# Kernel tuning notes

Hardware: AMD Instinct MI355X
Metric: run time of the kernel (lower is better)

Reference implementation:

```python
import jax, jax.numpy as jnp
import numpy as np

N_SRC0, N_DST0, N_DST1 = 100000, 50000, 25000
E0, E1, D = 1600000, 800000, 128


def setup_inputs() -> dict:
    key = jax.random.key(0)
    k = jax.random.split(key, 8)
    return {
        "x": jax.random.normal(k[0], (N_SRC0, D), dtype=jnp.float32),
        "src0": jax.random.randint(k[1], (E0,), 0, N_SRC0, dtype=jnp.int32),
        "dst0": jax.random.randint(k[2], (E0,), 0, N_DST0, dtype=jnp.int32),
        "ew0": jax.random.uniform(k[3], (E0,), dtype=jnp.float32),
        "src1": jax.random.randint(k[4], (E1,), 0, N_DST0, dtype=jnp.int32),
        "dst1": jax.random.randint(k[5], (E1,), 0, N_DST1, dtype=jnp.int32),
        "ew1": jax.random.uniform(k[6], (E1,), dtype=jnp.float32),
        "n_dst0": N_DST0,
        "n_dst1": N_DST1,
    }


def _propagate(h, src, dst, ew, n_dst):
    # u_mul_e: gather src feature per edge and scale by edge weight; sum-reduce to dst
    m = h[src] * ew[:, None]                      # [E, D]
    return jax.ops.segment_sum(m, dst, num_segments=n_dst)  # [n_dst, D]


def reference(x, src0, dst0, ew0, src1, dst1, ew1, n_dst0, n_dst1):
    # LightGCN forward over 2 sampled blocks, mlp_list=None
    h = _propagate(x, src0, dst0, ew0, n_dst0)    # [n_dst0, D]
    h = _propagate(h, src1, dst1, ew1, n_dst1)    # [n_dst1, D]
    return h
```

## Files before the change

kernel.cpp:

```cpp
#include <hip/hip_runtime.h>


#define DIMS 128
#define BK   64
#define BKSH 6
#define CAP  4096
#define CH   8192

__device__ __forceinline__ unsigned bf16_1(float a) {
  unsigned u = __float_as_uint(a);
  return (u + 0x7fffu + ((u >> 16) & 1u)) >> 16;
}

__device__ __forceinline__ int chunk_swz(int b, int NW) {
  const int q = NW >> 3, r = NW & 7, x = b & 7;
  return (x < r ? x * (q + 1) : r * (q + 1) + (x - r) * q) + (b >> 3);
}

__global__ __launch_bounds__(256) void hist_cvt(
    const int* __restrict__ dst0, const int* __restrict__ dst1,
    const float* __restrict__ xf, uint2* __restrict__ xq,
    float* __restrict__ xscale,
    int* __restrict__ wgcnt0, int* __restrict__ wgcnt1,
    int E0, int E1, int NB0, int NB1, int NW0, int NW1, int NSRC) {
  int b = blockIdx.x;
  if (b < NW0 + NW1) {
    __shared__ int hist[1024];
    const int s1 = (b >= NW0);
    const int w  = s1 ? chunk_swz(b - NW0, NW1) : chunk_swz(b, NW0);
    const int E  = s1 ? E1 : E0;
    const int NB = s1 ? NB1 : NB0;
    const int* dst = s1 ? dst1 : dst0;
    int* wgcnt = s1 ? wgcnt1 : wgcnt0;
    for (int i = threadIdx.x; i < NB; i += 256) hist[i] = 0;
    __syncthreads();
    const int beg = w * CH, end = min(beg + CH, E);
    for (int e = beg + threadIdx.x; e < end; e += 256)
      atomicAdd(&hist[dst[e] >> BKSH], 1);
    __syncthreads();
    for (int i = threadIdx.x; i < NB; i += 256)
      wgcnt[w * NB + i] = hist[i];
  } else {
    int gi = (b - NW0 - NW1) * 256 + threadIdx.x;
    int row = gi >> 4, c = gi & 15;
    if (row < NSRC) {
      const float4* xf4 = (const float4*)xf;
      float4 v0 = xf4[(size_t)row * 32 + c * 2];
      float4 v1 = xf4[(size_t)row * 32 + c * 2 + 1];
      float m = fmaxf(fmaxf(fmaxf(fabsf(v0.x), fabsf(v0.y)),
                            fmaxf(fabsf(v0.z), fabsf(v0.w))),
                      fmaxf(fmaxf(fabsf(v1.x), fabsf(v1.y)),
                            fmaxf(fabsf(v1.z), fabsf(v1.w))));
      m = fmaxf(m, __shfl_xor(m, 1));
      m = fmaxf(m, __shfl_xor(m, 2));
      m = fmaxf(m, __shfl_xor(m, 4));
      m = fmaxf(m, __shfl_xor(m, 8));
      float inv = (m > 0.f) ? 127.0f / m : 0.f;
      int q0 = (int)rintf(v0.x * inv), q1 = (int)rintf(v0.y * inv);
      int q2 = (int)rintf(v0.z * inv), q3 = (int)rintf(v0.w * inv);
      int q4 = (int)rintf(v1.x * inv), q5 = (int)rintf(v1.y * inv);
      int q6 = (int)rintf(v1.z * inv), q7 = (int)rintf(v1.w * inv);
      unsigned lo = (q0 & 255) | ((q1 & 255) << 8) |
                    ((q2 & 255) << 16) | ((q3 & 255) << 24);
      unsigned hi = (q4 & 255) | ((q5 & 255) << 8) |
                    ((q6 & 255) << 16) | ((q7 & 255) << 24);
      xq[(size_t)row * 16 + c] = make_uint2(lo, hi);
      if (c == 0) xscale[row] = m * (1.0f / 127.0f);
    }
  }
}

__global__ __launch_bounds__(256) void scan_cols(
    int* __restrict__ wgcnt0, int* __restrict__ wgcnt1,
    int* __restrict__ gcur, int2* __restrict__ rg0, int2* __restrict__ rg1,
    int NB0, int NB1, int NW0, int NW1) {
  __shared__ int part[256];
  int b = blockIdx.x;
  const int s1 = (b >= NB0);
  const int i = s1 ? b - NB0 : b;
  int* wgcnt = s1 ? wgcnt1 : wgcnt0;
  int2* rg   = s1 ? rg1 : rg0;
  const int NB = s1 ? NB1 : NB0;
  const int NW = s1 ? NW1 : NW0;
  const int t = threadIdx.x;
  int v = (t < NW) ? wgcnt[t * NB + i] : 0;
  part[t] = v;
  __syncthreads();
  for (int off = 1; off < 256; off <<= 1) {
    int u = (t >= off) ? part[t - off] : 0;
    __syncthreads();
    part[t] += u;
    __syncthreads();
  }
  if (t < NW) wgcnt[t * NB + i] = part[t] - v;
  if (t == 255) {
    int tot = part[255];
    int base = atomicAdd(&gcur[s1], tot);
    rg[i] = make_int2(base, base + tot);
  }
}

__global__ __launch_bounds__(512) void partition_k(
    const int* __restrict__ src0, const int* __restrict__ dst0,
    const float* __restrict__ ew0, const int* __restrict__ src1,
    const int* __restrict__ dst1, const float* __restrict__ ew1,
    const int* __restrict__ wgcnt0, const int* __restrict__ wgcnt1,
    const int2* __restrict__ rg0, const int2* __restrict__ rg1,
    int2* __restrict__ payl0, int2* __restrict__ payl1,
    int E0, int E1, int NB0, int NB1, int NW0, int NW1) {
  __shared__ int cur[1024];
  int b = blockIdx.x;
  const int s1 = (b >= NW0);
  const int w  = s1 ? chunk_swz(b - NW0, NW1) : chunk_swz(b, NW0);
  const int E  = s1 ? E1 : E0;
  const int NB = s1 ? NB1 : NB0;
  const int* src = s1 ? src1 : src0;
  const int* dst = s1 ? dst1 : dst0;
  const float* ew = s1 ? ew1 : ew0;
  const int* wgcnt = s1 ? wgcnt1 : wgcnt0;
  const int2* rg = s1 ? rg1 : rg0;
  int2* payl = s1 ? payl1 : payl0;
  for (int i = threadIdx.x; i < NB; i += 512)
    cur[i] = rg[i].x + wgcnt[w * NB + i];
  __syncthreads();
  const int beg = w * CH, end = min(beg + CH, E);
  for (int e = beg + threadIdx.x; e < end; e += 512) {
    int d = dst[e];
    int pos = atomicAdd(&cur[d >> BKSH], 1);
    payl[pos] = make_int2(src[e],
                          (int)((bf16_1(ew[e]) << 16) | (unsigned)(d & (BK - 1))));
  }
}

#define EDGE_BLOCK8(ws, u)                                      \
  {                                                             \
    a0 += (float)((int)((u).x << 24) >> 24) * (ws);             \
    a1 += (float)((int)((u).x << 16) >> 24) * (ws);             \
    a2 += (float)((int)((u).x << 8) >> 24) * (ws);              \
    a3 += (float)((int)(u).x >> 24) * (ws);                     \
    a4 += (float)((int)((u).y << 24) >> 24) * (ws);             \
    a5 += (float)((int)((u).y << 16) >> 24) * (ws);             \
    a6 += (float)((int)((u).y << 8) >> 24) * (ws);              \
    a7 += (float)((int)(u).y >> 24) * (ws);                     \
  }

template <bool OUT_I8>
__global__ __launch_bounds__(512) void gather_bkt(
    const uint2* __restrict__ feat, const float* __restrict__ scl,
    const int2* __restrict__ rg, const int2* __restrict__ payl,
    void* __restrict__ outp, float* __restrict__ oscale, int n_dst) {
  __shared__ int2 lp[CAP];
  __shared__ int cnt[BK], base[BK], cnt2[BK];
  const int b = blockIdx.x;
  const int tid = threadIdx.x;
  const int2 r = rg[b];
  const int n = r.y - r.x;
  const int nin = min(n, CAP);
  if (tid < BK) { cnt[tid] = 0; cnt2[tid] = 0; }
  __syncthreads();
  for (int j = tid; j < nin; j += 512)
    atomicAdd(&cnt[payl[r.x + j].y & (BK - 1)], 1);
  __syncthreads();
  if (tid < 64) {
    int v = cnt[tid];
    int s = v;
    for (int off = 1; off < 64; off <<= 1) {
      int u = __shfl_up(s, off);
      if (tid >= off) s += u;
    }
    base[tid] = s - v;
  }
  __syncthreads();
  for (int j = tid; j < nin; j += 512) {
    int2 p = payl[r.x + j];
    int dl = p.y & (BK - 1);
    float ws = __uint_as_float((unsigned)p.y & 0xffff0000u) * scl[p.x];
    int pos = base[dl] + atomicAdd(&cnt2[dl], 1);
    lp[pos] = make_int2(p.x, (int)((bf16_1(ws) << 16) | (unsigned)dl));
  }
  __syncthreads();
  const int wave = tid >> 6;
  const int lane = tid & 63;
  const int rr = lane >> 4;
  const int c  = lane & 15;
  for (int dl = wave; dl < BK; dl += 8) {
    const int row = b * BK + dl;
    if (row >= n_dst) break;
    const int bg = base[dl];
    const int en = bg + cnt[dl];
    float a0 = 0.f, a1 = 0.f, a2 = 0.f, a3 = 0.f;
    float a4 = 0.f, a5 = 0.f, a6 = 0.f, a7 = 0.f;
    for (int j = bg; j < en; j += 4) {
      int jj = j + rr;
      int2 p = (jj < en) ? lp[jj] : make_int2(0, 0);
      float ws = __uint_as_float((unsigned)p.y & 0xffff0000u);
      uint2 u = feat[(size_t)p.x * 16 + c];
      EDGE_BLOCK8(ws, u);
    }
    if (n > CAP) {
      for (int j = CAP; j < n; j += 4) {
        int jj = j + rr;
        int2 p = (jj < n) ? payl[r.x + jj] : make_int2(0, 0);
        bool mine = (jj < n) && ((p.y & (BK - 1)) == dl);
        float ws = mine
            ? __uint_as_float((unsigned)p.y & 0xffff0000u) * scl[p.x] : 0.f;
        uint2 u = feat[(size_t)p.x * 16 + c];
        EDGE_BLOCK8(ws, u);
      }
    }
    a0 += __shfl_xor(a0, 16); a0 += __shfl_xor(a0, 32);
    a1 += __shfl_xor(a1, 16); a1 += __shfl_xor(a1, 32);
    a2 += __shfl_xor(a2, 16); a2 += __shfl_xor(a2, 32);
    a3 += __shfl_xor(a3, 16); a3 += __shfl_xor(a3, 32);
    a4 += __shfl_xor(a4, 16); a4 += __shfl_xor(a4, 32);
    a5 += __shfl_xor(a5, 16); a5 += __shfl_xor(a5, 32);
    a6 += __shfl_xor(a6, 16); a6 += __shfl_xor(a6, 32);
    a7 += __shfl_xor(a7, 16); a7 += __shfl_xor(a7, 32);
    if (OUT_I8) {
      float m = fmaxf(fmaxf(fmaxf(fabsf(a0), fabsf(a1)),
                            fmaxf(fabsf(a2), fabsf(a3))),
                      fmaxf(fmaxf(fabsf(a4), fabsf(a5)),
                            fmaxf(fabsf(a6), fabsf(a7))));
      m = fmaxf(m, __shfl_xor(m, 1));
      m = fmaxf(m, __shfl_xor(m, 2));
      m = fmaxf(m, __shfl_xor(m, 4));
      m = fmaxf(m, __shfl_xor(m, 8));
      m = fmaxf(m, __shfl_xor(m, 16));
      m = fmaxf(m, __shfl_xor(m, 32));
      float inv = (m > 0.f) ? 127.0f / m : 0.f;
      if (rr == 0) {
        int q0 = (int)rintf(a0 * inv), q1 = (int)rintf(a1 * inv);
        int q2 = (int)rintf(a2 * inv), q3 = (int)rintf(a3 * inv);
        int q4 = (int)rintf(a4 * inv), q5 = (int)rintf(a5 * inv);
        int q6 = (int)rintf(a6 * inv), q7 = (int)rintf(a7 * inv);
        unsigned lo = (q0 & 255) | ((q1 & 255) << 8) |
                      ((q2 & 255) << 16) | ((q3 & 255) << 24);
        unsigned hi = (q4 & 255) | ((q5 & 255) << 8) |
                      ((q6 & 255) << 16) | ((q7 & 255) << 24);
        ((uint2*)outp)[(size_t)row * 16 + c] = make_uint2(lo, hi);
      }
      if (lane == 0) oscale[row] = m * (1.0f / 127.0f);
    } else {
      if (rr < 2) {
        ((float4*)outp)[(size_t)row * 32 + c * 2 + rr] =
            (rr == 0) ? make_float4(a0, a1, a2, a3)
                      : make_float4(a4, a5, a6, a7);
      }
    }
  }
}

#define COLG 32
__global__ __launch_bounds__(256) void prop_atomic(
    const float* __restrict__ x, const int* __restrict__ src,
    const int* __restrict__ dst, const float* __restrict__ ew,
    float* __restrict__ out, int E) {
  long long idx = (long long)blockIdx.x * blockDim.x + threadIdx.x;
  long long total = (long long)E * COLG;
  if (idx >= total) return;
  int e = (int)(idx >> 5);
  int cg = (int)(idx & 31);
  int s = src[e];
  int d = dst[e];
  float w = ew[e];
  const float4 v = *reinterpret_cast<const float4*>(x + (size_t)s * DIMS + cg * 4);
  float* o = out + (size_t)d * DIMS + cg * 4;
  atomicAdd(o + 0, v.x * w);
  atomicAdd(o + 1, v.y * w);
  atomicAdd(o + 2, v.z * w);
  atomicAdd(o + 3, v.w * w);
}


static inline size_t align_up(size_t v, size_t a) { return (v + a - 1) / a * a; }

extern "C" void kernel_launch(void* const* d_in, const int* in_sizes, int n_in,
                              void* d_out, int out_size, void* d_ws, size_t ws_size,
                              hipStream_t stream) {
  const float* x    = (const float*)d_in[0];
  const int*   src0 = (const int*)d_in[1];
  const int*   dst0 = (const int*)d_in[2];
  const float* ew0  = (const float*)d_in[3];
  const int*   src1 = (const int*)d_in[4];
  const int*   dst1 = (const int*)d_in[5];
  const float* ew1  = (const float*)d_in[6];

  const int N_SRC0 = in_sizes[0] / DIMS;
  const int E0 = in_sizes[1];
  const int E1 = in_sizes[4];
  const int N_DST0 = 50000;
  const int N_DST1 = 25000;

  const int NB0 = (N_DST0 + BK - 1) / BK;
  const int NB1 = (N_DST1 + BK - 1) / BK;
  const int NW0 = (E0 + CH - 1) / CH;
  const int NW1 = (E1 + CH - 1) / CH;

  float* out = (float*)d_out;

  char* ws = (char*)d_ws;
  size_t off = 0;
  uint2* xq     = (uint2*)(ws + off); off = align_up(off + (size_t)N_SRC0 * 16 * 8, 16);
  float* xscale = (float*)(ws + off); off = align_up(off + (size_t)N_SRC0 * 4, 16);
  uint2* hq     = (uint2*)(ws + off); off = align_up(off + (size_t)N_DST0 * 16 * 8, 16);
  float* hscale = (float*)(ws + off); off = align_up(off + (size_t)N_DST0 * 4, 16);
  int* wgcnt0   = (int*)(ws + off);   off = align_up(off + (size_t)NW0 * NB0 * 4, 16);
  int* wgcnt1   = (int*)(ws + off);   off = align_up(off + (size_t)NW1 * NB1 * 4, 16);
  int* gcur     = (int*)(ws + off);   off = align_up(off + 2 * 4, 16);
  int2* rg0     = (int2*)(ws + off);  off = align_up(off + (size_t)NB0 * 8, 16);
  int2* rg1     = (int2*)(ws + off);  off = align_up(off + (size_t)NB1 * 8, 16);
  int2* payl0   = (int2*)(ws + off);  off = align_up(off + (size_t)E0 * 8, 16);
  int2* payl1   = (int2*)(ws + off);  off = align_up(off + (size_t)E1 * 8, 16);
  const size_t needed = off;

  if (ws_size < needed) {
    float* h = (float*)d_ws;
    hipMemsetAsync(h, 0, (size_t)N_DST0 * DIMS * 4, stream);
    hipMemsetAsync(out, 0, (size_t)N_DST1 * DIMS * 4, stream);
    long long t0 = (long long)E0 * COLG;
    prop_atomic<<<(int)((t0 + 255) / 256), 256, 0, stream>>>(x, src0, dst0, ew0, h, E0);
    long long t1 = (long long)E1 * COLG;
    prop_atomic<<<(int)((t1 + 255) / 256), 256, 0, stream>>>(h, src1, dst1, ew1, out, E1);
    return;
  }

  const int cvtBlocks = (N_SRC0 * 16 + 255) / 256;

  hipMemsetAsync(gcur, 0, 2 * 4, stream);

  hist_cvt<<<NW0 + NW1 + cvtBlocks, 256, 0, stream>>>(
      dst0, dst1, x, xq, xscale, wgcnt0, wgcnt1,
      E0, E1, NB0, NB1, NW0, NW1, N_SRC0);

  scan_cols<<<NB0 + NB1, 256, 0, stream>>>(wgcnt0, wgcnt1, gcur, rg0, rg1,
                                           NB0, NB1, NW0, NW1);

  partition_k<<<NW0 + NW1, 512, 0, stream>>>(
      src0, dst0, ew0, src1, dst1, ew1, wgcnt0, wgcnt1, rg0, rg1,
      payl0, payl1, E0, E1, NB0, NB1, NW0, NW1);

  gather_bkt<true><<<NB0, 512, 0, stream>>>(
      xq, xscale, rg0, payl0, (void*)hq, hscale, N_DST0);

  gather_bkt<false><<<NB1, 512, 0, stream>>>(
      hq, hscale, rg1, payl1, (void*)out, (float*)nullptr, N_DST1);
}
```

Baseline: 169.3 us.

## Replace histogram-scan-partition with per-XCC fixed-capacity bucket cells and overflow list

Drops the three-pass counting sort (histogram, column scan, partition) and replaces it with a single scatter kernel. That kernel atomically appends each edge into a fixed-capacity cell indexed by XCC id and destination bucket, and spills any excess to a global overflow list. The source scale is folded into the edge weight at scatter time, and the source index is pre-multiplied by 16, so the gather no longer rescales. The goal is fewer launches and passes over the edge arrays, with global atomics kept within one XCC. In exchange there are global atomics per edge, a large padded workspace, and an overflow path that every bucket scans serially. That path gets expensive if cells overflow. Layer 1 scatter now depends on the layer 0 output scale, so the two layers' scatters are serialized.

```diff
diff --git a/kernel.cpp b/kernel.cpp
--- a/kernel.cpp
+++ b/kernel.cpp
@@ -4,131 +4,73 @@
 #define DIMS 128
 #define BK   64
 #define BKSH 6
-#define CAP  4096
-#define CH   8192
+#define CAPC 384
+#define LPC  (8 * CAPC)
 
 __device__ __forceinline__ unsigned bf16_1(float a) {
   unsigned u = __float_as_uint(a);
   return (u + 0x7fffu + ((u >> 16) & 1u)) >> 16;
 }
 
-__device__ __forceinline__ int chunk_swz(int b, int NW) {
-  const int q = NW >> 3, r = NW & 7, x = b & 7;
-  return (x < r ? x * (q + 1) : r * (q + 1) + (x - r) * q) + (b >> 3);
-}
-
-__global__ __launch_bounds__(256) void hist_cvt(
-    const int* __restrict__ dst0, const int* __restrict__ dst1,
+__device__ __forceinline__ int xcc_id() {
+  unsigned x;
+  asm volatile("s_getreg_b32 %0, hwreg(HW_REG_XCC_ID)" : "=s"(x));
+  return (int)(x & 7);
+}
+
+__global__ __launch_bounds__(256) void cvt_q(
     const float* __restrict__ xf, uint2* __restrict__ xq,
-    float* __restrict__ xscale,
-    int* __restrict__ wgcnt0, int* __restrict__ wgcnt1,
-    int E0, int E1, int NB0, int NB1, int NW0, int NW1, int NSRC) {
-  int b = blockIdx.x;
-  if (b < NW0 + NW1) {
-    __shared__ int hist[1024];
-    const int s1 = (b >= NW0);
-    const int w  = s1 ? chunk_swz(b - NW0, NW1) : chunk_swz(b, NW0);
-    const int E  = s1 ? E1 : E0;
-    const int NB = s1 ? NB1 : NB0;
-    const int* dst = s1 ? dst1 : dst0;
-    int* wgcnt = s1 ? wgcnt1 : wgcnt0;
-    for (int i = threadIdx.x; i < NB; i += 256) hist[i] = 0;
-    __syncthreads();
-    const int beg = w * CH, end = min(beg + CH, E);
-    for (int e = beg + threadIdx.x; e < end; e += 256)
-      atomicAdd(&hist[dst[e] >> BKSH], 1);
-    __syncthreads();
-    for (int i = threadIdx.x; i < NB; i += 256)
-      wgcnt[w * NB + i] = hist[i];
+    float* __restrict__ xscale, int NSRC) {
+  int gi = blockIdx.x * 256 + threadIdx.x;
+  int row = gi >> 4, c = gi & 15;
+  if (row >= NSRC) return;
+  const float4* xf4 = (const float4*)xf;
+  float4 v0 = xf4[(size_t)row * 32 + c * 2];
+  float4 v1 = xf4[(size_t)row * 32 + c * 2 + 1];
+  float m = fmaxf(fmaxf(fmaxf(fabsf(v0.x), fabsf(v0.y)),
+                        fmaxf(fabsf(v0.z), fabsf(v0.w))),
+                  fmaxf(fmaxf(fabsf(v1.x), fabsf(v1.y)),
+                        fmaxf(fabsf(v1.z), fabsf(v1.w))));
+  m = fmaxf(m, __shfl_xor(m, 1));
+  m = fmaxf(m, __shfl_xor(m, 2));
+  m = fmaxf(m, __shfl_xor(m, 4));
+  m = fmaxf(m, __shfl_xor(m, 8));
+  float inv = (m > 0.f) ? 127.0f / m : 0.f;
+  int q0 = (int)rintf(v0.x * inv), q1 = (int)rintf(v0.y * inv);
+  int q2 = (int)rintf(v0.z * inv), q3 = (int)rintf(v0.w * inv);
+  int q4 = (int)rintf(v1.x * inv), q5 = (int)rintf(v1.y * inv);
+  int q6 = (int)rintf(v1.z * inv), q7 = (int)rintf(v1.w * inv);
+  unsigned lo = (q0 & 255) | ((q1 & 255) << 8) |
+                ((q2 & 255) << 16) | ((q3 & 255) << 24);
+  unsigned hi = (q4 & 255) | ((q5 & 255) << 8) |
+                ((q6 & 255) << 16) | ((q7 & 255) << 24);
+  xq[(size_t)row * 16 + c] = make_uint2(lo, hi);
+  if (c == 0) xscale[row] = m * (1.0f / 127.0f);
+}
+
+__global__ __launch_bounds__(256) void scatter_cell(
+    const int* __restrict__ src, const int* __restrict__ dst,
+    const float* __restrict__ ew, const float* __restrict__ scl,
+    int* __restrict__ cur, int2* __restrict__ payl,
+    int* __restrict__ ovfc, int2* __restrict__ ovfp, int* __restrict__ ovfb,
+    int E, int NB) {
+  int e = blockIdx.x * 256 + threadIdx.x;
+  if (e >= E) return;
+  int x = xcc_id();
+  int d = dst[e];
+  int b = d >> BKSH;
+  int s = src[e];
+  float ws = ew[e] * scl[s];
+  int2 pv = make_int2(s << 4,
+                      (int)((bf16_1(ws) << 16) | (unsigned)(d & (BK - 1))));
+  int cell = x * NB + b;
+  int pos = atomicAdd(&cur[cell], 1);
+  if (pos < CAPC) {
+    payl[(size_t)cell * CAPC + pos] = pv;
   } else {
-    int gi = (b - NW0 - NW1) * 256 + threadIdx.x;
-    int row = gi >> 4, c = gi & 15;
-    if (row < NSRC) {
-      const float4* xf4 = (const float4*)xf;
-      float4 v0 = xf4[(size_t)row * 32 + c * 2];
-      float4 v1 = xf4[(size_t)row * 32 + c * 2 + 1];
-      float m = fmaxf(fmaxf(fmaxf(fabsf(v0.x), fabsf(v0.y)),
-                            fmaxf(fabsf(v0.z), fabsf(v0.w))),
-                      fmaxf(fmaxf(fabsf(v1.x), fabsf(v1.y)),
-                            fmaxf(fabsf(v1.z), fabsf(v1.w))));
-      m = fmaxf(m, __shfl_xor(m, 1));
-      m = fmaxf(m, __shfl_xor(m, 2));
-      m = fmaxf(m, __shfl_xor(m, 4));
-      m = fmaxf(m, __shfl_xor(m, 8));
-      float inv = (m > 0.f) ? 127.0f / m : 0.f;
-      int q0 = (int)rintf(v0.x * inv), q1 = (int)rintf(v0.y * inv);
-      int q2 = (int)rintf(v0.z * inv), q3 = (int)rintf(v0.w * inv);
-      int q4 = (int)rintf(v1.x * inv), q5 = (int)rintf(v1.y * inv);
-      int q6 = (int)rintf(v1.z * inv), q7 = (int)rintf(v1.w * inv);
-      unsigned lo = (q0 & 255) | ((q1 & 255) << 8) |
-                    ((q2 & 255) << 16) | ((q3 & 255) << 24);
-      unsigned hi = (q4 & 255) | ((q5 & 255) << 8) |
-                    ((q6 & 255) << 16) | ((q7 & 255) << 24);
-      xq[(size_t)row * 16 + c] = make_uint2(lo, hi);
-      if (c == 0) xscale[row] = m * (1.0f / 127.0f);
-    }
-  }
-}
-
-__global__ __launch_bounds__(256) void scan_cols(
-    int* __restrict__ wgcnt0, int* __restrict__ wgcnt1,
-    int* __restrict__ gcur, int2* __restrict__ rg0, int2* __restrict__ rg1,
-    int NB0, int NB1, int NW0, int NW1) {
-  __shared__ int part[256];
-  int b = blockIdx.x;
-  const int s1 = (b >= NB0);
-  const int i = s1 ? b - NB0 : b;
-  int* wgcnt = s1 ? wgcnt1 : wgcnt0;
-  int2* rg   = s1 ? rg1 : rg0;
-  const int NB = s1 ? NB1 : NB0;
-  const int NW = s1 ? NW1 : NW0;
-  const int t = threadIdx.x;
-  int v = (t < NW) ? wgcnt[t * NB + i] : 0;
-  part[t] = v;
-  __syncthreads();
-  for (int off = 1; off < 256; off <<= 1) {
-    int u = (t >= off) ? part[t - off] : 0;
-    __syncthreads();
-    part[t] += u;
-    __syncthreads();
-  }
-  if (t < NW) wgcnt[t * NB + i] = part[t] - v;
-  if (t == 255) {
-    int tot = part[255];
-    int base = atomicAdd(&gcur[s1], tot);
-    rg[i] = make_int2(base, base + tot);
-  }
-}
-
-__global__ __launch_bounds__(512) void partition_k(
-    const int* __restrict__ src0, const int* __restrict__ dst0,
-    const float* __restrict__ ew0, const int* __restrict__ src1,
-    const int* __restrict__ dst1, const float* __restrict__ ew1,
-    const int* __restrict__ wgcnt0, const int* __restrict__ wgcnt1,
-    const int2* __restrict__ rg0, const int2* __restrict__ rg1,
-    int2* __restrict__ payl0, int2* __restrict__ payl1,
-    int E0, int E1, int NB0, int NB1, int NW0, int NW1) {
-  __shared__ int cur[1024];
-  int b = blockIdx.x;
-  const int s1 = (b >= NW0);
-  const int w  = s1 ? chunk_swz(b - NW0, NW1) : chunk_swz(b, NW0);
-  const int E  = s1 ? E1 : E0;
-  const int NB = s1 ? NB1 : NB0;
-  const int* src = s1 ? src1 : src0;
-  const int* dst = s1 ? dst1 : dst0;
-  const float* ew = s1 ? ew1 : ew0;
-  const int* wgcnt = s1 ? wgcnt1 : wgcnt0;
-  const int2* rg = s1 ? rg1 : rg0;
-  int2* payl = s1 ? payl1 : payl0;
-  for (int i = threadIdx.x; i < NB; i += 512)
-    cur[i] = rg[i].x + wgcnt[w * NB + i];
-  __syncthreads();
-  const int beg = w * CH, end = min(beg + CH, E);
-  for (int e = beg + threadIdx.x; e < end; e += 512) {
-    int d = dst[e];
-    int pos = atomicAdd(&cur[d >> BKSH], 1);
-    payl[pos] = make_int2(src[e],
-                          (int)((bf16_1(ew[e]) << 16) | (unsigned)(d & (BK - 1))));
+    int o = atomicAdd(ovfc, 1);
+    ovfp[o] = pv;
+    ovfb[o] = b;
   }
 }
 
@@ -145,21 +87,25 @@
   }
 
 template <bool OUT_I8>
-__global__ __launch_bounds__(512) void gather_bkt(
-    const uint2* __restrict__ feat, const float* __restrict__ scl,
-    const int2* __restrict__ rg, const int2* __restrict__ payl,
-    void* __restrict__ outp, float* __restrict__ oscale, int n_dst) {
-  __shared__ int2 lp[CAP];
+__global__ __launch_bounds__(512) void gather_cell(
+    const uint2* __restrict__ feat, const int* __restrict__ cur,
+    const int2* __restrict__ payl, const int* __restrict__ ovfc,
+    const int2* __restrict__ ovfp, const int* __restrict__ ovfb,
+    void* __restrict__ outp, float* __restrict__ oscale, int n_dst, int NB) {
+  __shared__ int2 lp[LPC];
   __shared__ int cnt[BK], base[BK], cnt2[BK];
+  __shared__ int segc[8];
   const int b = blockIdx.x;
   const int tid = threadIdx.x;
-  const int2 r = rg[b];
-  const int n = r.y - r.x;
-  const int nin = min(n, CAP);
   if (tid < BK) { cnt[tid] = 0; cnt2[tid] = 0; }
-  __syncthreads();
-  for (int j = tid; j < nin; j += 512)
-    atomicAdd(&cnt[payl[r.x + j].y & (BK - 1)], 1);
+  if (tid < 8) segc[tid] = min(cur[tid * NB + b], CAPC);
+  __syncthreads();
+  for (int x = 0; x < 8; ++x) {
+    const int n = segc[x];
+    const int2* sp = payl + (size_t)(x * NB + b) * CAPC;
+    for (int j = tid; j < n; j += 512)
+      atomicAdd(&cnt[sp[j].y & (BK - 1)], 1);
+  }
   __syncthreads();
   if (tid < 64) {
     int v = cnt[tid];
@@ -171,14 +117,17 @@
     base[tid] = s - v;
   }
   __syncthreads();
-  for (int j = tid; j < nin; j += 512) {
-    int2 p = payl[r.x + j];
-    int dl = p.y & (BK - 1);
-    float ws = __uint_as_float((unsigned)p.y & 0xffff0000u) * scl[p.x];
-    int pos = base[dl] + atomicAdd(&cnt2[dl], 1);
-    lp[pos] = make_int2(p.x, (int)((bf16_1(ws) << 16) | (unsigned)dl));
-  }
-  __syncthreads();
+  for (int x = 0; x < 8; ++x) {
+    const int n = segc[x];
+    const int2* sp = payl + (size_t)(x * NB + b) * CAPC;
+    for (int j = tid; j < n; j += 512) {
+      int2 p = sp[j];
+      int dl = p.y & (BK - 1);
+      lp[base[dl] + atomicAdd(&cnt2[dl], 1)] = p;
+    }
+  }
+  __syncthreads();
+  const int novf = *ovfc;
   const int wave = tid >> 6;
   const int lane = tid & 63;
   const int rr = lane >> 4;
@@ -194,17 +143,17 @@
       int jj = j + rr;
       int2 p = (jj < en) ? lp[jj] : make_int2(0, 0);
       float ws = __uint_as_float((unsigned)p.y & 0xffff0000u);
-      uint2 u = feat[(size_t)p.x * 16 + c];
+      uint2 u = feat[(size_t)p.x + c];
       EDGE_BLOCK8(ws, u);
     }
-    if (n > CAP) {
-      for (int j = CAP; j < n; j += 4) {
+    if (novf > 0) {
+      for (int j = 0; j < novf; j += 4) {
         int jj = j + rr;
-        int2 p = (jj < n) ? payl[r.x + jj] : make_int2(0, 0);
-        bool mine = (jj < n) && ((p.y & (BK - 1)) == dl);
-        float ws = mine
-            ? __uint_as_float((unsigned)p.y & 0xffff0000u) * scl[p.x] : 0.f;
-        uint2 u = feat[(size_t)p.x * 16 + c];
+        bool in = (jj < novf);
+        int2 p = in ? ovfp[jj] : make_int2(0, 0);
+        bool mine = in && (ovfb[jj] == b) && ((p.y & (BK - 1)) == dl);
+        float ws = mine ? __uint_as_float((unsigned)p.y & 0xffff0000u) : 0.f;
+        uint2 u = feat[(size_t)p.x + c];
         EDGE_BLOCK8(ws, u);
       }
     }
@@ -293,8 +242,6 @@
 
   const int NB0 = (N_DST0 + BK - 1) / BK;
   const int NB1 = (N_DST1 + BK - 1) / BK;
-  const int NW0 = (E0 + CH - 1) / CH;
-  const int NW1 = (E1 + CH - 1) / CH;
 
   float* out = (float*)d_out;
 
@@ -304,13 +251,15 @@
   float* xscale = (float*)(ws + off); off = align_up(off + (size_t)N_SRC0 * 4, 16);
   uint2* hq     = (uint2*)(ws + off); off = align_up(off + (size_t)N_DST0 * 16 * 8, 16);
   float* hscale = (float*)(ws + off); off = align_up(off + (size_t)N_DST0 * 4, 16);
-  int* wgcnt0   = (int*)(ws + off);   off = align_up(off + (size_t)NW0 * NB0 * 4, 16);
-  int* wgcnt1   = (int*)(ws + off);   off = align_up(off + (size_t)NW1 * NB1 * 4, 16);
-  int* gcur     = (int*)(ws + off);   off = align_up(off + 2 * 4, 16);
-  int2* rg0     = (int2*)(ws + off);  off = align_up(off + (size_t)NB0 * 8, 16);
-  int2* rg1     = (int2*)(ws + off);  off = align_up(off + (size_t)NB1 * 8, 16);
-  int2* payl0   = (int2*)(ws + off);  off = align_up(off + (size_t)E0 * 8, 16);
-  int2* payl1   = (int2*)(ws + off);  off = align_up(off + (size_t)E1 * 8, 16);
+  int* cur0     = (int*)(ws + off);   off = align_up(off + (size_t)8 * NB0 * 4, 16);
+  int* cur1     = (int*)(ws + off);   off = align_up(off + (size_t)8 * NB1 * 4, 16);
+  int* ovfc     = (int*)(ws + off);   off = align_up(off + 2 * 4, 16);
+  int2* payl0   = (int2*)(ws + off);  off = align_up(off + (size_t)8 * NB0 * CAPC * 8, 16);
+  int2* payl1   = (int2*)(ws + off);  off = align_up(off + (size_t)8 * NB1 * CAPC * 8, 16);
+  int2* ovfp0   = (int2*)(ws + off);  off = align_up(off + (size_t)E0 * 8, 16);
+  int* ovfb0    = (int*)(ws + off);   off = align_up(off + (size_t)E0 * 4, 16);
+  int2* ovfp1   = (int2*)(ws + off);  off = align_up(off + (size_t)E1 * 8, 16);
+  int* ovfb1    = (int*)(ws + off);   off = align_up(off + (size_t)E1 * 4, 16);
   const size_t needed = off;
 
   if (ws_size < needed) {
@@ -324,24 +273,22 @@
     return;
   }
 
-  const int cvtBlocks = (N_SRC0 * 16 + 255) / 256;
-
-  hipMemsetAsync(gcur, 0, 2 * 4, stream);
-
-  hist_cvt<<<NW0 + NW1 + cvtBlocks, 256, 0, stream>>>(
-      dst0, dst1, x, xq, xscale, wgcnt0, wgcnt1,
-      E0, E1, NB0, NB1, NW0, NW1, N_SRC0);
-
-  scan_cols<<<NB0 + NB1, 256, 0, stream>>>(wgcnt0, wgcnt1, gcur, rg0, rg1,
-                                           NB0, NB1, NW0, NW1);
-
-  partition_k<<<NW0 + NW1, 512, 0, stream>>>(
-      src0, dst0, ew0, src1, dst1, ew1, wgcnt0, wgcnt1, rg0, rg1,
-      payl0, payl1, E0, E1, NB0, NB1, NW0, NW1);
-
-  gather_bkt<true><<<NB0, 512, 0, stream>>>(
-      xq, xscale, rg0, payl0, (void*)hq, hscale, N_DST0);
-
-  gather_bkt<false><<<NB1, 512, 0, stream>>>(
-      hq, hscale, rg1, payl1, (void*)out, (float*)nullptr, N_DST1);
-}
+  hipMemsetAsync(cur0, 0, (size_t)8 * NB0 * 4, stream);
+  hipMemsetAsync(cur1, 0, (size_t)8 * NB1 * 4, stream);
+  hipMemsetAsync(ovfc, 0, 2 * 4, stream);
+
+  cvt_q<<<(N_SRC0 * 16 + 255) / 256, 256, 0, stream>>>(x, xq, xscale, N_SRC0);
+
+  scatter_cell<<<(E0 + 255) / 256, 256, 0, stream>>>(
+      src0, dst0, ew0, xscale, cur0, payl0, &ovfc[0], ovfp0, ovfb0, E0, NB0);
+
+  gather_cell<true><<<NB0, 512, 0, stream>>>(
+      xq, cur0, payl0, &ovfc[0], ovfp0, ovfb0, (void*)hq, hscale, N_DST0, NB0);
+
+  scatter_cell<<<(E1 + 255) / 256, 256, 0, stream>>>(
+      src1, dst1, ew1, hscale, cur1, payl1, &ovfc[1], ovfp1, ovfb1, E1, NB1);
+
+  gather_cell<false><<<NB1, 512, 0, stream>>>(
+      hq, cur1, payl1, &ovfc[1], ovfp1, ovfb1, (void*)out, (float*)nullptr,
+      N_DST1, NB1);
+}
```

New measurement: 281.2 us. 66.1% more time.
